# Optimization experiments

Measured on AMD Instinct MI355X. Metric: run time of the kernel, lower is better.

## Reference

```python
import jax, jax.numpy as jnp
import numpy as np

N, E, F_IN, EF, HID = 100000, 1600000, 32, 8, 16


def gat_conv(x, W, att_src, att_dst, b, src, dst, heads, out_ch):
    # PyG GATConv: h = x@W per head; score = LeakyReLU(a_s.h_src + a_d.h_dst);
    # segment-softmax over incoming edges of each dst; weighted sum of h_src.
    n = x.shape[0]
    h = (x @ W).reshape(n, heads, out_ch)                      # [N,H,C]
    a_s = jnp.sum(h * att_src, axis=-1)                        # [N,H]
    a_d = jnp.sum(h * att_dst, axis=-1)                        # [N,H]
    e = jax.nn.leaky_relu(a_s[src] + a_d[dst], 0.2)            # [E',H]
    m = jax.ops.segment_max(e, dst, num_segments=n)            # [N,H]
    ex = jnp.exp(e - m[dst])
    denom = jax.ops.segment_sum(ex, dst, num_segments=n)
    alpha = ex / (denom[dst] + 1e-16)                          # [E',H]
    out = jax.ops.segment_sum(h[src] * alpha[:, :, None], dst, num_segments=n)
    return out.reshape(n, heads * out_ch) + b


def setup_inputs() -> dict:
    key = jax.random.key(0)
    ks = jax.random.split(key, 16)
    s = 0.1
    return {
        "x": jax.random.normal(ks[0], (N, F_IN), jnp.float32),
        "edge_index": jax.random.randint(ks[1], (2, E), 0, N, jnp.int32),
        "edge_attr": jax.random.uniform(ks[2], (E, 2 * EF), jnp.float32),
        "num_edge_features": EF,
        "num_edge_masks": EF,
        # conv1: heads=4, out=16
        "W1": jax.random.normal(ks[3], (F_IN, 4 * HID), jnp.float32) * s,
        "att_src1": jax.random.normal(ks[4], (4, HID), jnp.float32) * s,
        "att_dst1": jax.random.normal(ks[5], (4, HID), jnp.float32) * s,
        "b1": jnp.zeros((4 * HID,), jnp.float32),
        # conv2: heads=1, out=16
        "W2": jax.random.normal(ks[6], (4 * HID, HID), jnp.float32) * s,
        "att_src2": jax.random.normal(ks[7], (1, HID), jnp.float32) * s,
        "att_dst2": jax.random.normal(ks[8], (1, HID), jnp.float32) * s,
        "b2": jnp.zeros((HID,), jnp.float32),
        # edge MLP
        "mlp_W1": jax.random.normal(ks[9], (EF, HID), jnp.float32) * s,
        "mlp_b1": jnp.zeros((HID,), jnp.float32),
        "mlp_W2": jax.random.normal(ks[10], (HID, HID), jnp.float32) * s,
        "mlp_b2": jnp.zeros((HID,), jnp.float32),
        # fc_edge: 3*hid -> 1
        "fc_W": jax.random.normal(ks[11], (3 * HID, 1), jnp.float32) * s,
        "fc_b": jnp.zeros((1,), jnp.float32),
    }


def reference(x, edge_index, edge_attr, num_edge_features, num_edge_masks,
              W1, att_src1, att_dst1, b1, W2, att_src2, att_dst2, b2,
              mlp_W1, mlp_b1, mlp_W2, mlp_b2, fc_W, fc_b):
    n = x.shape[0]
    src, dst = edge_index[0], edge_index[1]
    # GATConv adds self loops internally (PyG default)
    loops = jnp.arange(n, dtype=edge_index.dtype)
    src_sl = jnp.concatenate([src, loops])
    dst_sl = jnp.concatenate([dst, loops])
    ef = edge_attr[:, :num_edge_features] * edge_attr[:, num_edge_features:]
    h = gat_conv(x, W1, att_src1, att_dst1, b1, src_sl, dst_sl, 4, HID)
    h = jax.nn.elu(h)                                          # dropout: eval mode -> identity
    h = gat_conv(h, W2, att_src2, att_dst2, b2, src_sl, dst_sl, 1, HID)
    ef = jax.nn.relu(ef @ mlp_W1 + mlp_b1) @ mlp_W2 + mlp_b2   # edge MLP
    emb = jnp.concatenate([h[src], h[dst], ef], axis=1)        # [E,3*HID]
    return (emb @ fc_W + fc_b).squeeze(-1)                     # [E]
```

## Files before the change

kernel.cpp:

```cpp
#include <hip/hip_runtime.h>
#include <hip/hip_bf16.h>
#include <hip/hip_fp16.h>


#define FIN 32
#define C1 64
#define HID 16
#define BSH 8
#define CAP2 6144

__device__ __forceinline__ float leaky02(float x) {
    return x > 0.f ? x : 0.2f * x;
}

__global__ void k_binit3(int* __restrict__ bcur, int nbuck) {
    int b = blockIdx.x * blockDim.x + threadIdx.x;
    if (b < nbuck) bcur[b] = b * CAP2;
}

__global__ void __launch_bounds__(256) k_bin(
        const int* __restrict__ src, const int* __restrict__ dst,
        int* __restrict__ bcur, unsigned* __restrict__ brec,
        int e, int ep, int nbuck) {
    __shared__ int hist[512];
    __shared__ int sc[2][512];
    __shared__ int bstart[512];
    __shared__ int off2[512];
    __shared__ int gbase[512];
    __shared__ unsigned srec[4096];
    __shared__ unsigned short sbkt[4096];
    int tid = threadIdx.x;
    int cb = blockIdx.x * 4096;
    int cnt = min(4096, ep - cb);
    for (int j = tid; j < 512; j += 256) hist[j] = 0;
    __syncthreads();
    unsigned rec[16];
    int bk[16];
#pragma unroll
    for (int t = 0; t < 16; t++) {
        int i = cb + t * 256 + tid;
        bk[t] = -1;
        if (i < ep) {
            int s, d;
            if (i < e) { s = src[i]; d = dst[i]; }
            else       { s = i - e; d = s; }
            int b = d >> BSH;
            rec[t] = ((unsigned)(d & 255) << 17) | (unsigned)s;
            bk[t] = b;
            atomicAdd(&hist[b], 1);
        }
    }
    __syncthreads();
    for (int j = tid; j < 512; j += 256) sc[0][j] = hist[j];
    __syncthreads();
    int pi = 0;
    for (int off = 1; off < 512; off <<= 1) {
        int po = pi ^ 1;
        for (int j = tid; j < 512; j += 256)
            sc[po][j] = sc[pi][j] + ((j >= off) ? sc[pi][j - off] : 0);
        __syncthreads();
        pi = po;
    }
    for (int j = tid; j < 512; j += 256) {
        int excl = sc[pi][j] - hist[j];
        bstart[j] = excl;
        off2[j] = excl;
    }
    __syncthreads();
    for (int b = tid; b < nbuck; b += 256) {
        int c = hist[b];
        if (c > 0) gbase[b] = atomicAdd(&bcur[b], c);
    }
    __syncthreads();
#pragma unroll
    for (int t = 0; t < 16; t++) {
        if (bk[t] >= 0) {
            int p = atomicAdd(&off2[bk[t]], 1);
            srec[p] = rec[t];
            sbkt[p] = (unsigned short)bk[t];
        }
    }
    __syncthreads();
    for (int i = tid; i < cnt; i += 256) {
        int b = sbkt[i];
        int idx = gbase[b] + (i - bstart[b]);
        if (idx < (b + 1) * CAP2)
            brec[idx] = srec[i];
    }
}

__global__ void __launch_bounds__(256) k_fine2(
        const unsigned* __restrict__ brec, const int* __restrict__ bcur,
        int* __restrict__ offs, int* __restrict__ oend,
        int* __restrict__ ssrc, int n) {
    __shared__ int lcnt[256];
    __shared__ int sbuf[256];
    __shared__ unsigned stage[CAP2];
    __shared__ int sorted[CAP2];
    int b = blockIdx.x;
    int n0 = b << BSH;
    int tid = threadIdx.x;
    int base = b * CAP2;
    int cnt = min(bcur[b] - base, CAP2);
    lcnt[tid] = 0;
    __syncthreads();
    for (int i = tid; i < cnt; i += 256) {
        unsigned r = brec[base + i];
        stage[i] = r;
        atomicAdd(&lcnt[r >> 17], 1);
    }
    __syncthreads();
    int v = lcnt[tid];
    sbuf[tid] = v;
    __syncthreads();
    for (int off = 1; off < 256; off <<= 1) {
        int u = (tid >= off) ? sbuf[tid - off] : 0;
        __syncthreads();
        sbuf[tid] += u;
        __syncthreads();
    }
    int excl = sbuf[tid] - v;
    if (n0 + tid < n) {
        offs[n0 + tid] = base + excl;
        oend[n0 + tid] = base + excl + v;
    }
    lcnt[tid] = excl;
    __syncthreads();
    for (int i = tid; i < cnt; i += 256) {
        unsigned r = stage[i];
        int p = atomicAdd(&lcnt[r >> 17], 1);
        sorted[p] = (int)(r & 0x1FFFF);
    }
    __syncthreads();
    for (int i = tid; i < cnt; i += 256) ssrc[base + i] = sorted[i];
}

__global__ void k_node1(const float* __restrict__ x, const float* __restrict__ W1,
                        const float* __restrict__ att_s, const float* __restrict__ att_d,
                        __half* __restrict__ h1h, float* __restrict__ a1, float* __restrict__ d1,
                        int n) {
    __shared__ float sW[FIN * C1];
    __shared__ float sA[C1], sD[C1];
    __shared__ float sX[4 * FIN];
    int t = threadIdx.x;
    for (int i = t; i < FIN * C1; i += 256) sW[i] = W1[i];
    if (t < C1) { sA[t] = att_s[t]; sD[t] = att_d[t]; }
    int base = blockIdx.x * 4;
    if (t < 4 * FIN) {
        int nn = base + (t >> 5);
        sX[t] = (nn < n) ? x[(size_t)nn * FIN + (t & 31)] : 0.f;
    }
    __syncthreads();
    int li = t >> 6;
    int c  = t & 63;
    int node = base + li;
    if (node >= n) return;
    const float* xr = sX + li * FIN;
    float acc = 0.f;
#pragma unroll
    for (int k = 0; k < FIN; k++) acc += xr[k] * sW[k * C1 + c];
    h1h[(size_t)node * C1 + c] = __float2half(acc);
    float pa = acc * sA[c], pb = acc * sD[c];
#pragma unroll
    for (int m = 8; m >= 1; m >>= 1) {
        pa += __shfl_xor(pa, m, 16);
        pb += __shfl_xor(pb, m, 16);
    }
    if ((c & 15) == 0) {
        a1[node * 4 + (c >> 4)] = pa;
        d1[node * 4 + (c >> 4)] = pb;
    }
}

__global__ void __launch_bounds__(256) k_agg1(
        const __half* __restrict__ h1h, const float* __restrict__ a1,
        const float* __restrict__ d1, const float* __restrict__ b1,
        const int* __restrict__ offs, const int* __restrict__ oend,
        const int* __restrict__ ssrc,
        float* __restrict__ out1, int n) {
    __shared__ float4 w4l[4][64];
    __shared__ int    sil[4][64];
    int wid = (int)((blockIdx.x * (size_t)blockDim.x + threadIdx.x) >> 6);
    int lane = threadIdx.x & 63;
    int wl = threadIdx.x >> 6;
    int which = lane >> 5;
    int lane32 = lane & 31;
    int node = wid * 2 + which;
    if (node >= n) return;
    int sub = lane32 & 7;
    int g   = lane32 >> 3;
    int head = sub >> 1;
    unsigned lane_off = (unsigned)sub * 16u;
    const char* hb = (const char*)h1h;
    float4 dv = ((const float4*)d1)[node];
    int s0 = offs[node], s1v = oend[node];
    float acc[8] = {0.f, 0.f, 0.f, 0.f, 0.f, 0.f, 0.f, 0.f};
    float dsum = 0.f;
    for (int base = s0; base < s1v; base += 32) {
        int cnt = min(32, s1v - base);
        int sl = (lane32 < cnt) ? ssrc[base + lane32] : 0;
        float4 a4 = ((const float4*)a1)[(unsigned)sl];
        float4 w4;
        if (lane32 < cnt) {
            w4.x = __expf(leaky02(a4.x + dv.x));
            w4.y = __expf(leaky02(a4.y + dv.y));
            w4.z = __expf(leaky02(a4.z + dv.z));
            w4.w = __expf(leaky02(a4.w + dv.w));
        } else {
            w4.x = w4.y = w4.z = w4.w = 0.f;
        }
        w4l[wl][lane] = w4;
        sil[wl][lane] = sl;
        __builtin_amdgcn_wave_barrier();
        int cnt4 = (cnt + 3) & ~3;
        int lbase = which << 5;
#pragma unroll 2
        for (int j = g; j < cnt4; j += 4) {
            int s   = sil[wl][lbase + j];
            float w = ((const float*)&w4l[wl][lbase + j])[head];
            float4 raw = *(const float4*)(hb + (((unsigned)s) << 7) + lane_off);
            float2 f0 = __half22float2(*(__half2*)&raw.x);
            float2 f1 = __half22float2(*(__half2*)&raw.y);
            float2 f2 = __half22float2(*(__half2*)&raw.z);
            float2 f3 = __half22float2(*(__half2*)&raw.w);
            acc[0] = fmaf(w, f0.x, acc[0]);
            acc[1] = fmaf(w, f0.y, acc[1]);
            acc[2] = fmaf(w, f1.x, acc[2]);
            acc[3] = fmaf(w, f1.y, acc[3]);
            acc[4] = fmaf(w, f2.x, acc[4]);
            acc[5] = fmaf(w, f2.y, acc[5]);
            acc[6] = fmaf(w, f3.x, acc[6]);
            acc[7] = fmaf(w, f3.y, acc[7]);
            dsum += w;
        }
        __builtin_amdgcn_wave_barrier();
    }
#pragma unroll
    for (int m = 8; m <= 16; m <<= 1) {
#pragma unroll
        for (int i = 0; i < 8; i++) acc[i] += __shfl_xor(acc[i], m, 64);
        dsum += __shfl_xor(dsum, m, 64);
    }
    if (lane32 < 8) {
        float inv = 1.f / (dsum + 1e-16f);
        float4 bA = ((const float4*)b1)[lane32 * 2];
        float4 bB = ((const float4*)b1)[lane32 * 2 + 1];
        float4 oA, oB;
        oA.x = acc[0] * inv + bA.x;  oA.x = oA.x > 0.f ? oA.x : expm1f(oA.x);
        oA.y = acc[1] * inv + bA.y;  oA.y = oA.y > 0.f ? oA.y : expm1f(oA.y);
        oA.z = acc[2] * inv + bA.z;  oA.z = oA.z > 0.f ? oA.z : expm1f(oA.z);
        oA.w = acc[3] * inv + bA.w;  oA.w = oA.w > 0.f ? oA.w : expm1f(oA.w);
        oB.x = acc[4] * inv + bB.x;  oB.x = oB.x > 0.f ? oB.x : expm1f(oB.x);
        oB.y = acc[5] * inv + bB.y;  oB.y = oB.y > 0.f ? oB.y : expm1f(oB.y);
        oB.z = acc[6] * inv + bB.z;  oB.z = oB.z > 0.f ? oB.z : expm1f(oB.z);
        oB.w = acc[7] * inv + bB.w;  oB.w = oB.w > 0.f ? oB.w : expm1f(oB.w);
        ((float4*)out1)[(size_t)node * 16 + lane32 * 2]     = oA;
        ((float4*)out1)[(size_t)node * 16 + lane32 * 2 + 1] = oB;
    }
}

__global__ void k_node2(const float* __restrict__ out1, const float* __restrict__ W2,
                        const float* __restrict__ att_s2, const float* __restrict__ att_d2,
                        __half* __restrict__ h2h, float* __restrict__ a2, float* __restrict__ d2,
                        int n) {
    __shared__ float sW[C1 * HID];
    __shared__ float sX[16 * 65];
    int t = threadIdx.x;
    for (int i = t; i < C1 * HID; i += 256) sW[i] = W2[i];
    int base = blockIdx.x * 16;
    for (int i = t; i < 16 * C1; i += 256) {
        int nn = base + (i >> 6);
        sX[(i >> 6) * 65 + (i & 63)] = (nn < n) ? out1[(size_t)nn * C1 + (i & 63)] : 0.f;
    }
    __syncthreads();
    int li = t >> 4, c = t & 15;
    int node = base + li;
    if (node >= n) return;
    float acc = 0.f;
#pragma unroll
    for (int k = 0; k < C1; k++) acc += sX[li * 65 + k] * sW[k * HID + c];
    h2h[(size_t)node * HID + c] = __float2half(acc);
    float pa = acc * att_s2[c], pb = acc * att_d2[c];
#pragma unroll
    for (int m = 8; m >= 1; m >>= 1) {
        pa += __shfl_xor(pa, m, 16);
        pb += __shfl_xor(pb, m, 16);
    }
    if (c == 0) { a2[node] = pa; d2[node] = pb; }
}

__global__ void __launch_bounds__(256) k_agg2(
        const __half* __restrict__ h2h, const float* __restrict__ a2,
        const float* __restrict__ d2, const float* __restrict__ b2,
        const float* __restrict__ fcW,
        const int* __restrict__ offs, const int* __restrict__ oend,
        const int* __restrict__ ssrc,
        float* __restrict__ ps, float* __restrict__ pd, int n) {
    __shared__ float2 wsl[4][64];
    int wid = (int)((blockIdx.x * (size_t)blockDim.x + threadIdx.x) >> 6);
    int lane = threadIdx.x & 63;
    int wl = threadIdx.x >> 6;
    int which = lane >> 5;
    int lane32 = lane & 31;
    int node = wid * 2 + which;
    if (node >= n) return;
    int sub = lane32 & 1;
    int g   = lane32 >> 1;
    unsigned lane_off = (unsigned)sub * 16u;
    const char* hb = (const char*)h2h;
    float dvv = d2[node];
    int s0 = offs[node], s1v = oend[node];
    float acc[8] = {0.f, 0.f, 0.f, 0.f, 0.f, 0.f, 0.f, 0.f};
    float dsum = 0.f;
    for (int base = s0; base < s1v; base += 32) {
        int cnt = min(32, s1v - base);
        int sl = (lane32 < cnt) ? ssrc[base + lane32] : 0;
        float av = a2[(unsigned)sl];
        float w = (lane32 < cnt) ? __expf(leaky02(av + dvv)) : 0.f;
        wsl[wl][lane] = make_float2(w, __int_as_float(sl));
        __builtin_amdgcn_wave_barrier();
        int cnt16 = (cnt + 15) & ~15;
        int lbase = which << 5;
#pragma unroll 2
        for (int j = g; j < cnt16; j += 16) {
            float2 e0 = wsl[wl][lbase + j];
            int s = __float_as_int(e0.y);
            float4 raw = *(const float4*)(hb + (((unsigned)s) << 5) + lane_off);
            float2 f0 = __half22float2(*(__half2*)&raw.x);
            float2 f1 = __half22float2(*(__half2*)&raw.y);
            float2 f2 = __half22float2(*(__half2*)&raw.z);
            float2 f3 = __half22float2(*(__half2*)&raw.w);
            acc[0] = fmaf(e0.x, f0.x, acc[0]);
            acc[1] = fmaf(e0.x, f0.y, acc[1]);
            acc[2] = fmaf(e0.x, f1.x, acc[2]);
            acc[3] = fmaf(e0.x, f1.y, acc[3]);
            acc[4] = fmaf(e0.x, f2.x, acc[4]);
            acc[5] = fmaf(e0.x, f2.y, acc[5]);
            acc[6] = fmaf(e0.x, f3.x, acc[6]);
            acc[7] = fmaf(e0.x, f3.y, acc[7]);
            dsum += e0.x;
        }
        __builtin_amdgcn_wave_barrier();
    }
#pragma unroll
    for (int m = 2; m <= 16; m <<= 1) {
#pragma unroll
        for (int i = 0; i < 8; i++) acc[i] += __shfl_xor(acc[i], m, 64);
        dsum += __shfl_xor(dsum, m, 64);
    }
    float p1 = 0.f, p2 = 0.f;
    if (lane32 < 2) {
        float inv = 1.f / (dsum + 1e-16f);
        float4 bA = ((const float4*)b2)[lane32 * 2];
        float4 bB = ((const float4*)b2)[lane32 * 2 + 1];
        float4 fsA = ((const float4*)fcW)[lane32 * 2];
        float4 fsB = ((const float4*)fcW)[lane32 * 2 + 1];
        float4 fdA = ((const float4*)fcW)[4 + lane32 * 2];
        float4 fdB = ((const float4*)fcW)[4 + lane32 * 2 + 1];
        float h0 = acc[0] * inv + bA.x, h1v = acc[1] * inv + bA.y;
        float h2v = acc[2] * inv + bA.z, h3 = acc[3] * inv + bA.w;
        float h4 = acc[4] * inv + bB.x, h5 = acc[5] * inv + bB.y;
        float h6 = acc[6] * inv + bB.z, h7 = acc[7] * inv + bB.w;
        p1 = h0 * fsA.x + h1v * fsA.y + h2v * fsA.z + h3 * fsA.w
           + h4 * fsB.x + h5 * fsB.y + h6 * fsB.z + h7 * fsB.w;
        p2 = h0 * fdA.x + h1v * fdA.y + h2v * fdA.z + h3 * fdA.w
           + h4 * fdB.x + h5 * fdB.y + h6 * fdB.z + h7 * fdB.w;
    }
    p1 += __shfl_xor(p1, 1, 64);
    p2 += __shfl_xor(p2, 1, 64);
    if (lane32 == 0) { ps[node] = p1; pd[node] = p2; }
}

__global__ void k_edge_final(const float* __restrict__ ea, const int* __restrict__ src,
                             const int* __restrict__ dst, const float* __restrict__ ps,
                             const float* __restrict__ pd, const float* __restrict__ mlpW1,
                             const float* __restrict__ mlpb1,
                             const float* __restrict__ mlpW2, const float* __restrict__ mlpb2,
                             const float* __restrict__ fcW, const float* __restrict__ fcb,
                             float* __restrict__ out, int e) {
    __shared__ float sW[8 * 16];
    __shared__ float sb[16];
    __shared__ float sw2[17];
    int t = threadIdx.x;
    if (t < 128) sW[t] = mlpW1[t];
    if (t < 16)  sb[t] = mlpb1[t];
    if (t < 16) {
        float s = 0.f;
#pragma unroll
        for (int k = 0; k < 16; k++) s += mlpW2[t * 16 + k] * fcW[32 + k];
        sw2[t] = s;
    } else if (t == 16) {
        float s = fcb[0];
        for (int k = 0; k < 16; k++) s += mlpb2[k] * fcW[32 + k];
        sw2[16] = s;
    }
    __syncthreads();
    int eid = blockIdx.x * blockDim.x + t;
    if (eid >= e) return;
    const float4* ev = (const float4*)(ea) + (size_t)eid * 4;
    float4 v0 = ev[0], v1 = ev[1], v2 = ev[2], v3 = ev[3];
    float ef[8] = { v0.x * v2.x, v0.y * v2.y, v0.z * v2.z, v0.w * v2.w,
                    v1.x * v3.x, v1.y * v3.y, v1.z * v3.z, v1.w * v3.w };
    float acc = sw2[16];
#pragma unroll
    for (int j = 0; j < 16; j++) {
        float tt = sb[j];
#pragma unroll
        for (int i = 0; i < 8; i++) tt += ef[i] * sW[i * 16 + j];
        acc += fmaxf(tt, 0.f) * sw2[j];
    }
    out[eid] = acc + ps[src[eid]] + pd[dst[eid]];
}

extern "C" void kernel_launch(void* const* d_in, const int* in_sizes, int n_in,
                              void* d_out, int out_size, void* d_ws, size_t ws_size,
                              hipStream_t stream) {
    const float* x        = (const float*)d_in[0];
    const int*   eidx     = (const int*)d_in[1];
    const float* eattr    = (const float*)d_in[2];
    const float* W1       = (const float*)d_in[5];
    const float* att_s1   = (const float*)d_in[6];
    const float* att_d1   = (const float*)d_in[7];
    const float* b1       = (const float*)d_in[8];
    const float* W2       = (const float*)d_in[9];
    const float* att_s2   = (const float*)d_in[10];
    const float* att_d2   = (const float*)d_in[11];
    const float* b2       = (const float*)d_in[12];
    const float* mlp_W1   = (const float*)d_in[13];
    const float* mlp_b1   = (const float*)d_in[14];
    const float* mlp_W2   = (const float*)d_in[15];
    const float* mlp_b2   = (const float*)d_in[16];
    const float* fc_W     = (const float*)d_in[17];
    const float* fc_b     = (const float*)d_in[18];

    const int n = in_sizes[0] / FIN;
    const int e = in_sizes[2] / 16;
    const int ep = e + n;
    const int* src = eidx;
    const int* dst = eidx + e;
    const int nbuck = (n + 255) >> BSH;

    char* p = (char*)d_ws;
    auto carve = [&](size_t bytes) {
        char* r = p;
        p += (bytes + 255) & ~(size_t)255;
        return r;
    };
    __half* h1h  = (__half*)carve((size_t)n * C1 * 2);
    float*  out1 = (float*)carve((size_t)n * C1 * 4);
    __half* h2h  = (__half*)carve((size_t)n * HID * 2);
    float*  a1   = (float*)carve((size_t)n * 4 * 4);
    float*  d1   = (float*)carve((size_t)n * 4 * 4);
    float*  a2   = (float*)carve((size_t)n * 4);
    float*  d2   = (float*)carve((size_t)n * 4);
    float*  ps   = (float*)carve((size_t)n * 4);
    float*  pd   = (float*)carve((size_t)n * 4);
    int*    offs = (int*)carve((size_t)n * 4);
    int*    oendp= (int*)carve((size_t)n * 4);
    int*    bcur = (int*)carve(512 * 4);
    int*    ssrc = (int*)carve((size_t)nbuck * CAP2 * 4);
    unsigned* brec = (unsigned*)carve((size_t)nbuck * CAP2 * 4);

    float* outp = (float*)d_out;

    k_binit3<<<2, 256, 0, stream>>>(bcur, nbuck);
    k_bin<<<(ep + 4095) / 4096, 256, 0, stream>>>(src, dst, bcur, brec, e, ep, nbuck);
    k_fine2<<<nbuck, 256, 0, stream>>>(brec, bcur, offs, oendp, ssrc, n);

    k_node1<<<(n + 3) / 4, 256, 0, stream>>>(x, W1, att_s1, att_d1, h1h, a1, d1, n);
    {
        int npair = (n + 1) / 2;
        k_agg1<<<(npair * 64 + 255) / 256, 256, 0, stream>>>(h1h, a1, d1, b1, offs, oendp, ssrc, out1, n);
    }

    k_node2<<<(n + 15) / 16, 256, 0, stream>>>(out1, W2, att_s2, att_d2, h2h, a2, d2, n);
    {
        int npair = (n + 1) / 2;
        k_agg2<<<(npair * 64 + 255) / 256, 256, 0, stream>>>(h2h, a2, d2, b2, fc_W, offs, oendp, ssrc, ps, pd, n);
    }

    k_edge_final<<<(e + 255) / 256, 256, 0, stream>>>(eattr, src, dst, ps, pd,
                                                      mlp_W1, mlp_b1, mlp_W2, mlp_b2,
                                                      fc_W, fc_b, outp, e);
}
```

Measured before the change: 201.0 us.

## Co-schedule independent kernels and fuse node2 transform into layer-1 aggregation

Runs the edge MLP in the same launch as the binning pass and node1's linear transform in the same launch as the fine sort, using block-index ranges to split the work. Folds the layer-2 linear projection into the layer-1 aggregation epilogue through shared memory, so the float out1 buffer is never written to or read from global memory. Simplifies binning by dropping the shared-memory local sort before the global scatter, and the fine sort now scatters straight to global memory. The final edge kernel becomes a small gather-add onto the precomputed MLP output. In exchange, writes are less coalesced and the combined blocks are heterogeneous.

```diff
diff --git a/kernel.cpp b/kernel.cpp
--- a/kernel.cpp
+++ b/kernel.cpp
@@ -18,171 +18,183 @@
     if (b < nbuck) bcur[b] = b * CAP2;
 }
 
-__global__ void __launch_bounds__(256) k_bin(
+__global__ void __launch_bounds__(256) k_binF(
         const int* __restrict__ src, const int* __restrict__ dst,
         int* __restrict__ bcur, unsigned* __restrict__ brec,
-        int e, int ep, int nbuck) {
-    __shared__ int hist[512];
-    __shared__ int sc[2][512];
-    __shared__ int bstart[512];
-    __shared__ int off2[512];
-    __shared__ int gbase[512];
-    __shared__ unsigned srec[4096];
-    __shared__ unsigned short sbkt[4096];
+        const float* __restrict__ ea,
+        const float* __restrict__ mlpW1, const float* __restrict__ mlpb1,
+        const float* __restrict__ mlpW2, const float* __restrict__ mlpb2,
+        const float* __restrict__ fcW, const float* __restrict__ fcb,
+        float* __restrict__ outp,
+        int e, int ep, int nbuck, int gbin) {
+    __shared__ int cnt[512];
+    __shared__ int cur[512];
+    __shared__ float sW[128];
+    __shared__ float sb[16];
+    __shared__ float sw2[17];
     int tid = threadIdx.x;
-    int cb = blockIdx.x * 4096;
-    int cnt = min(4096, ep - cb);
-    for (int j = tid; j < 512; j += 256) hist[j] = 0;
-    __syncthreads();
-    unsigned rec[16];
-    int bk[16];
-#pragma unroll
-    for (int t = 0; t < 16; t++) {
-        int i = cb + t * 256 + tid;
-        bk[t] = -1;
-        if (i < ep) {
-            int s, d;
-            if (i < e) { s = src[i]; d = dst[i]; }
-            else       { s = i - e; d = s; }
-            int b = d >> BSH;
-            rec[t] = ((unsigned)(d & 255) << 17) | (unsigned)s;
-            bk[t] = b;
-            atomicAdd(&hist[b], 1);
-        }
-    }
-    __syncthreads();
-    for (int j = tid; j < 512; j += 256) sc[0][j] = hist[j];
-    __syncthreads();
-    int pi = 0;
-    for (int off = 1; off < 512; off <<= 1) {
-        int po = pi ^ 1;
-        for (int j = tid; j < 512; j += 256)
-            sc[po][j] = sc[pi][j] + ((j >= off) ? sc[pi][j - off] : 0);
-        __syncthreads();
-        pi = po;
-    }
-    for (int j = tid; j < 512; j += 256) {
-        int excl = sc[pi][j] - hist[j];
-        bstart[j] = excl;
-        off2[j] = excl;
-    }
-    __syncthreads();
-    for (int b = tid; b < nbuck; b += 256) {
-        int c = hist[b];
-        if (c > 0) gbase[b] = atomicAdd(&bcur[b], c);
-    }
-    __syncthreads();
-#pragma unroll
-    for (int t = 0; t < 16; t++) {
-        if (bk[t] >= 0) {
-            int p = atomicAdd(&off2[bk[t]], 1);
-            srec[p] = rec[t];
-            sbkt[p] = (unsigned short)bk[t];
-        }
-    }
-    __syncthreads();
-    for (int i = tid; i < cnt; i += 256) {
-        int b = sbkt[i];
-        int idx = gbase[b] + (i - bstart[b]);
-        if (idx < (b + 1) * CAP2)
-            brec[idx] = srec[i];
-    }
-}
-
-__global__ void __launch_bounds__(256) k_fine2(
+    if ((int)blockIdx.x < gbin) {
+        int cb = blockIdx.x * 4096;
+        for (int j = tid; j < 512; j += 256) cnt[j] = 0;
+        __syncthreads();
+        unsigned rec[16];
+        int bk[16];
+#pragma unroll
+        for (int t = 0; t < 16; t++) {
+            int i = cb + t * 256 + tid;
+            bk[t] = -1;
+            if (i < ep) {
+                int s, d;
+                if (i < e) { s = src[i]; d = dst[i]; }
+                else       { s = i - e; d = s; }
+                int b = d >> BSH;
+                rec[t] = ((unsigned)(d & 255) << 17) | (unsigned)s;
+                bk[t] = b;
+                atomicAdd(&cnt[b], 1);
+            }
+        }
+        __syncthreads();
+        for (int b = tid; b < nbuck; b += 256) {
+            int c = cnt[b];
+            cur[b] = (c > 0) ? atomicAdd(&bcur[b], c) : 0;
+        }
+        __syncthreads();
+#pragma unroll
+        for (int t = 0; t < 16; t++) {
+            if (bk[t] >= 0) {
+                int p = atomicAdd(&cur[bk[t]], 1);
+                if (p < (bk[t] + 1) * CAP2)
+                    brec[p] = rec[t];
+            }
+        }
+    } else {
+        if (tid < 128) sW[tid] = mlpW1[tid];
+        if (tid < 16)  sb[tid] = mlpb1[tid];
+        if (tid < 16) {
+            float s = 0.f;
+#pragma unroll
+            for (int k = 0; k < 16; k++) s += mlpW2[tid * 16 + k] * fcW[32 + k];
+            sw2[tid] = s;
+        } else if (tid == 16) {
+            float s = fcb[0];
+            for (int k = 0; k < 16; k++) s += mlpb2[k] * fcW[32 + k];
+            sw2[16] = s;
+        }
+        __syncthreads();
+        int eid = ((int)blockIdx.x - gbin) * 256 + tid;
+        if (eid >= e) return;
+        const float4* ev = (const float4*)ea + (size_t)eid * 4;
+        float4 v0 = ev[0], v1 = ev[1], v2 = ev[2], v3 = ev[3];
+        float ef[8] = { v0.x * v2.x, v0.y * v2.y, v0.z * v2.z, v0.w * v2.w,
+                        v1.x * v3.x, v1.y * v3.y, v1.z * v3.z, v1.w * v3.w };
+        float acc = sw2[16];
+#pragma unroll
+        for (int j = 0; j < 16; j++) {
+            float tt = sb[j];
+#pragma unroll
+            for (int i = 0; i < 8; i++) tt += ef[i] * sW[i * 16 + j];
+            acc += fmaxf(tt, 0.f) * sw2[j];
+        }
+        outp[eid] = acc;
+    }
+}
+
+__global__ void __launch_bounds__(256) k_fineF(
         const unsigned* __restrict__ brec, const int* __restrict__ bcur,
-        int* __restrict__ offs, int* __restrict__ oend,
-        int* __restrict__ ssrc, int n) {
+        int* __restrict__ offs, int* __restrict__ oend, int* __restrict__ ssrc,
+        const float* __restrict__ x, const float* __restrict__ W1,
+        const float* __restrict__ att_s, const float* __restrict__ att_d,
+        __half* __restrict__ h1h, float* __restrict__ a1, float* __restrict__ d1,
+        int n, int gfine) {
     __shared__ int lcnt[256];
     __shared__ int sbuf[256];
-    __shared__ unsigned stage[CAP2];
-    __shared__ int sorted[CAP2];
-    int b = blockIdx.x;
-    int n0 = b << BSH;
-    int tid = threadIdx.x;
-    int base = b * CAP2;
-    int cnt = min(bcur[b] - base, CAP2);
-    lcnt[tid] = 0;
-    __syncthreads();
-    for (int i = tid; i < cnt; i += 256) {
-        unsigned r = brec[base + i];
-        stage[i] = r;
-        atomicAdd(&lcnt[r >> 17], 1);
-    }
-    __syncthreads();
-    int v = lcnt[tid];
-    sbuf[tid] = v;
-    __syncthreads();
-    for (int off = 1; off < 256; off <<= 1) {
-        int u = (tid >= off) ? sbuf[tid - off] : 0;
-        __syncthreads();
-        sbuf[tid] += u;
-        __syncthreads();
-    }
-    int excl = sbuf[tid] - v;
-    if (n0 + tid < n) {
-        offs[n0 + tid] = base + excl;
-        oend[n0 + tid] = base + excl + v;
-    }
-    lcnt[tid] = excl;
-    __syncthreads();
-    for (int i = tid; i < cnt; i += 256) {
-        unsigned r = stage[i];
-        int p = atomicAdd(&lcnt[r >> 17], 1);
-        sorted[p] = (int)(r & 0x1FFFF);
-    }
-    __syncthreads();
-    for (int i = tid; i < cnt; i += 256) ssrc[base + i] = sorted[i];
-}
-
-__global__ void k_node1(const float* __restrict__ x, const float* __restrict__ W1,
-                        const float* __restrict__ att_s, const float* __restrict__ att_d,
-                        __half* __restrict__ h1h, float* __restrict__ a1, float* __restrict__ d1,
-                        int n) {
     __shared__ float sW[FIN * C1];
     __shared__ float sA[C1], sD[C1];
     __shared__ float sX[4 * FIN];
-    int t = threadIdx.x;
-    for (int i = t; i < FIN * C1; i += 256) sW[i] = W1[i];
-    if (t < C1) { sA[t] = att_s[t]; sD[t] = att_d[t]; }
-    int base = blockIdx.x * 4;
-    if (t < 4 * FIN) {
-        int nn = base + (t >> 5);
-        sX[t] = (nn < n) ? x[(size_t)nn * FIN + (t & 31)] : 0.f;
-    }
-    __syncthreads();
-    int li = t >> 6;
-    int c  = t & 63;
-    int node = base + li;
-    if (node >= n) return;
-    const float* xr = sX + li * FIN;
-    float acc = 0.f;
-#pragma unroll
-    for (int k = 0; k < FIN; k++) acc += xr[k] * sW[k * C1 + c];
-    h1h[(size_t)node * C1 + c] = __float2half(acc);
-    float pa = acc * sA[c], pb = acc * sD[c];
-#pragma unroll
-    for (int m = 8; m >= 1; m >>= 1) {
-        pa += __shfl_xor(pa, m, 16);
-        pb += __shfl_xor(pb, m, 16);
-    }
-    if ((c & 15) == 0) {
-        a1[node * 4 + (c >> 4)] = pa;
-        d1[node * 4 + (c >> 4)] = pb;
-    }
-}
-
-__global__ void __launch_bounds__(256) k_agg1(
+    int tid = threadIdx.x;
+    if ((int)blockIdx.x < gfine) {
+        int b = blockIdx.x;
+        int n0 = b << BSH;
+        int base = b * CAP2;
+        int cnt = min(bcur[b] - base, CAP2);
+        lcnt[tid] = 0;
+        __syncthreads();
+        for (int i = tid; i < cnt; i += 256) {
+            unsigned r = brec[base + i];
+            atomicAdd(&lcnt[r >> 17], 1);
+        }
+        __syncthreads();
+        int v = lcnt[tid];
+        sbuf[tid] = v;
+        __syncthreads();
+        for (int off = 1; off < 256; off <<= 1) {
+            int u = (tid >= off) ? sbuf[tid - off] : 0;
+            __syncthreads();
+            sbuf[tid] += u;
+            __syncthreads();
+        }
+        int excl = sbuf[tid] - v;
+        if (n0 + tid < n) {
+            offs[n0 + tid] = base + excl;
+            oend[n0 + tid] = base + excl + v;
+        }
+        lcnt[tid] = base + excl;
+        __syncthreads();
+        for (int i = tid; i < cnt; i += 256) {
+            unsigned r = brec[base + i];
+            int p = atomicAdd(&lcnt[r >> 17], 1);
+            ssrc[p] = (int)(r & 0x1FFFF);
+        }
+    } else {
+        int nb = (int)blockIdx.x - gfine;
+        for (int i = tid; i < FIN * C1; i += 256) sW[i] = W1[i];
+        if (tid < C1) { sA[tid] = att_s[tid]; sD[tid] = att_d[tid]; }
+        int bse = nb * 4;
+        if (tid < 4 * FIN) {
+            int nn = bse + (tid >> 5);
+            sX[tid] = (nn < n) ? x[(size_t)nn * FIN + (tid & 31)] : 0.f;
+        }
+        __syncthreads();
+        int li = tid >> 6, c = tid & 63;
+        int node = bse + li;
+        if (node >= n) return;
+        const float* xr = sX + li * FIN;
+        float acc = 0.f;
+#pragma unroll
+        for (int k = 0; k < FIN; k++) acc += xr[k] * sW[k * C1 + c];
+        h1h[(size_t)node * C1 + c] = __float2half(acc);
+        float pa = acc * sA[c], pb = acc * sD[c];
+#pragma unroll
+        for (int m = 8; m >= 1; m >>= 1) {
+            pa += __shfl_xor(pa, m, 16);
+            pb += __shfl_xor(pb, m, 16);
+        }
+        if ((c & 15) == 0) {
+            a1[node * 4 + (c >> 4)] = pa;
+            d1[node * 4 + (c >> 4)] = pb;
+        }
+    }
+}
+
+__global__ void __launch_bounds__(256) k_agg1F(
         const __half* __restrict__ h1h, const float* __restrict__ a1,
         const float* __restrict__ d1, const float* __restrict__ b1,
+        const float* __restrict__ W2,
+        const float* __restrict__ att_s2, const float* __restrict__ att_d2,
         const int* __restrict__ offs, const int* __restrict__ oend,
         const int* __restrict__ ssrc,
-        float* __restrict__ out1, int n) {
+        __half* __restrict__ h2h, float* __restrict__ a2, float* __restrict__ d2,
+        int n) {
     __shared__ float4 w4l[4][64];
     __shared__ int    sil[4][64];
-    int wid = (int)((blockIdx.x * (size_t)blockDim.x + threadIdx.x) >> 6);
-    int lane = threadIdx.x & 63;
-    int wl = threadIdx.x >> 6;
+    __shared__ float  sO[4][2][64];
+    __shared__ float  sW2[C1 * HID];
+    int tid = threadIdx.x;
+    for (int i = tid; i < C1 * HID; i += 256) sW2[i] = W2[i];
+    __syncthreads();
+    int wid = (int)((blockIdx.x * (size_t)blockDim.x + tid) >> 6);
+    int lane = tid & 63;
+    int wl = tid >> 6;
     int which = lane >> 5;
     int lane32 = lane & 31;
     int node = wid * 2 + which;
@@ -254,39 +266,25 @@
         oB.y = acc[5] * inv + bB.y;  oB.y = oB.y > 0.f ? oB.y : expm1f(oB.y);
         oB.z = acc[6] * inv + bB.z;  oB.z = oB.z > 0.f ? oB.z : expm1f(oB.z);
         oB.w = acc[7] * inv + bB.w;  oB.w = oB.w > 0.f ? oB.w : expm1f(oB.w);
-        ((float4*)out1)[(size_t)node * 16 + lane32 * 2]     = oA;
-        ((float4*)out1)[(size_t)node * 16 + lane32 * 2 + 1] = oB;
-    }
-}
-
-__global__ void k_node2(const float* __restrict__ out1, const float* __restrict__ W2,
-                        const float* __restrict__ att_s2, const float* __restrict__ att_d2,
-                        __half* __restrict__ h2h, float* __restrict__ a2, float* __restrict__ d2,
-                        int n) {
-    __shared__ float sW[C1 * HID];
-    __shared__ float sX[16 * 65];
-    int t = threadIdx.x;
-    for (int i = t; i < C1 * HID; i += 256) sW[i] = W2[i];
-    int base = blockIdx.x * 16;
-    for (int i = t; i < 16 * C1; i += 256) {
-        int nn = base + (i >> 6);
-        sX[(i >> 6) * 65 + (i & 63)] = (nn < n) ? out1[(size_t)nn * C1 + (i & 63)] : 0.f;
-    }
-    __syncthreads();
-    int li = t >> 4, c = t & 15;
-    int node = base + li;
-    if (node >= n) return;
-    float acc = 0.f;
-#pragma unroll
-    for (int k = 0; k < C1; k++) acc += sX[li * 65 + k] * sW[k * HID + c];
-    h2h[(size_t)node * HID + c] = __float2half(acc);
-    float pa = acc * att_s2[c], pb = acc * att_d2[c];
+        *((float4*)&sO[wl][which][lane32 * 8])     = oA;
+        *((float4*)&sO[wl][which][lane32 * 8 + 4]) = oB;
+    }
+    __builtin_amdgcn_wave_barrier();
+    int c = lane32 & 15, kh = lane32 >> 4;
+    const float* orow = sO[wl][which];
+    float part = 0.f;
+#pragma unroll
+    for (int k = 0; k < 32; k++)
+        part += orow[kh * 32 + k] * sW2[(kh * 32 + k) * HID + c];
+    part += __shfl_xor(part, 16, 64);
+    if (lane32 < 16) h2h[(size_t)node * HID + c] = __float2half(part);
+    float pa = part * att_s2[c], pb = part * att_d2[c];
 #pragma unroll
     for (int m = 8; m >= 1; m >>= 1) {
-        pa += __shfl_xor(pa, m, 16);
-        pb += __shfl_xor(pb, m, 16);
-    }
-    if (c == 0) { a2[node] = pa; d2[node] = pb; }
+        pa += __shfl_xor(pa, m, 64);
+        pb += __shfl_xor(pb, m, 64);
+    }
+    if (lane32 == 0) { a2[node] = pa; d2[node] = pb; }
 }
 
 __global__ void __launch_bounds__(256) k_agg2(
@@ -371,45 +369,12 @@
     if (lane32 == 0) { ps[node] = p1; pd[node] = p2; }
 }
 
-__global__ void k_edge_final(const float* __restrict__ ea, const int* __restrict__ src,
-                             const int* __restrict__ dst, const float* __restrict__ ps,
-                             const float* __restrict__ pd, const float* __restrict__ mlpW1,
-                             const float* __restrict__ mlpb1,
-                             const float* __restrict__ mlpW2, const float* __restrict__ mlpb2,
-                             const float* __restrict__ fcW, const float* __restrict__ fcb,
-                             float* __restrict__ out, int e) {
-    __shared__ float sW[8 * 16];
-    __shared__ float sb[16];
-    __shared__ float sw2[17];
-    int t = threadIdx.x;
-    if (t < 128) sW[t] = mlpW1[t];
-    if (t < 16)  sb[t] = mlpb1[t];
-    if (t < 16) {
-        float s = 0.f;
-#pragma unroll
-        for (int k = 0; k < 16; k++) s += mlpW2[t * 16 + k] * fcW[32 + k];
-        sw2[t] = s;
-    } else if (t == 16) {
-        float s = fcb[0];
-        for (int k = 0; k < 16; k++) s += mlpb2[k] * fcW[32 + k];
-        sw2[16] = s;
-    }
-    __syncthreads();
-    int eid = blockIdx.x * blockDim.x + t;
-    if (eid >= e) return;
-    const float4* ev = (const float4*)(ea) + (size_t)eid * 4;
-    float4 v0 = ev[0], v1 = ev[1], v2 = ev[2], v3 = ev[3];
-    float ef[8] = { v0.x * v2.x, v0.y * v2.y, v0.z * v2.z, v0.w * v2.w,
-                    v1.x * v3.x, v1.y * v3.y, v1.z * v3.z, v1.w * v3.w };
-    float acc = sw2[16];
-#pragma unroll
-    for (int j = 0; j < 16; j++) {
-        float tt = sb[j];
-#pragma unroll
-        for (int i = 0; i < 8; i++) tt += ef[i] * sW[i * 16 + j];
-        acc += fmaxf(tt, 0.f) * sw2[j];
-    }
-    out[eid] = acc + ps[src[eid]] + pd[dst[eid]];
+__global__ void __launch_bounds__(256) k_final2(
+        const int* __restrict__ src, const int* __restrict__ dst,
+        const float* __restrict__ ps, const float* __restrict__ pd,
+        float* __restrict__ out, int e) {
+    int eid = blockIdx.x * blockDim.x + threadIdx.x;
+    if (eid < e) out[eid] += ps[src[eid]] + pd[dst[eid]];
 }
 
 extern "C" void kernel_launch(void* const* d_in, const int* in_sizes, int n_in,
@@ -447,7 +412,6 @@
         return r;
     };
     __half* h1h  = (__half*)carve((size_t)n * C1 * 2);
-    float*  out1 = (float*)carve((size_t)n * C1 * 4);
     __half* h2h  = (__half*)carve((size_t)n * HID * 2);
     float*  a1   = (float*)carve((size_t)n * 4 * 4);
     float*  d1   = (float*)carve((size_t)n * 4 * 4);
@@ -463,23 +427,21 @@
 
     float* outp = (float*)d_out;
 
+    const int gbin  = (ep + 4095) / 4096;
+    const int gmlp  = (e + 255) / 256;
+    const int gnode1 = (n + 3) / 4;
+    const int npair = (n + 1) / 2;
+
     k_binit3<<<2, 256, 0, stream>>>(bcur, nbuck);
-    k_bin<<<(ep + 4095) / 4096, 256, 0, stream>>>(src, dst, bcur, brec, e, ep, nbuck);
-    k_fine2<<<nbuck, 256, 0, stream>>>(brec, bcur, offs, oendp, ssrc, n);
-
-    k_node1<<<(n + 3) / 4, 256, 0, stream>>>(x, W1, att_s1, att_d1, h1h, a1, d1, n);
-    {
-        int npair = (n + 1) / 2;
-        k_agg1<<<(npair * 64 + 255) / 256, 256, 0, stream>>>(h1h, a1, d1, b1, offs, oendp, ssrc, out1, n);
-    }
-
-    k_node2<<<(n + 15) / 16, 256, 0, stream>>>(out1, W2, att_s2, att_d2, h2h, a2, d2, n);
-    {
-        int npair = (n + 1) / 2;
-        k_agg2<<<(npair * 64 + 255) / 256, 256, 0, stream>>>(h2h, a2, d2, b2, fc_W, offs, oendp, ssrc, ps, pd, n);
-    }
-
-    k_edge_final<<<(e + 255) / 256, 256, 0, stream>>>(eattr, src, dst, ps, pd,
-                                                      mlp_W1, mlp_b1, mlp_W2, mlp_b2,
-                                                      fc_W, fc_b, outp, e);
-}
+    k_binF<<<gbin + gmlp, 256, 0, stream>>>(src, dst, bcur, brec, eattr,
+                                            mlp_W1, mlp_b1, mlp_W2, mlp_b2,
+                                            fc_W, fc_b, outp, e, ep, nbuck, gbin);
+    k_fineF<<<nbuck + gnode1, 256, 0, stream>>>(brec, bcur, offs, oendp, ssrc,
+                                                x, W1, att_s1, att_d1,
+                                                h1h, a1, d1, n, nbuck);
+    k_agg1F<<<(npair * 64 + 255) / 256, 256, 0, stream>>>(
+        h1h, a1, d1, b1, W2, att_s2, att_d2, offs, oendp, ssrc, h2h, a2, d2, n);
+    k_agg2<<<(npair * 64 + 255) / 256, 256, 0, stream>>>(
+        h2h, a2, d2, b2, fc_W, offs, oendp, ssrc, ps, pd, n);
+    k_final2<<<(e + 255) / 256, 256, 0, stream>>>(src, dst, ps, pd, outp, e);
+}
```

Result: faster. 183.9 us (-8.5%).
